# Kernel optimization log

Measured on AMD Instinct MI355X. Metric: run time of the kernel, lower is better.

Reference implementation:

```python
import jax, jax.numpy as jnp
import numpy as np

K_FRAC = 0.5  # matches init kwarg k


def setup_inputs() -> dict:
    key = jax.random.key(0)
    g = jax.random.normal(key, (16, 2048, 2048), dtype=jnp.float32)
    return {"g": g}


def reference(g):
    # k = int(N * k_frac): number of SMALLEST entries per row to zero out
    N = g.shape[-1]
    k = int(N * K_FRAC)
    g2 = g.reshape(-1, N)                       # [R, N]
    # indices of the k smallest values per row (topk of -g)
    _, idx = jax.lax.top_k(-g2, k)              # [R, k] int32
    rows = jnp.arange(g2.shape[0])[:, None]     # [R, 1]
    t = g2.at[rows, idx].set(0.0)               # scatter zeros at bottom-k positions
    return t.reshape(g.shape)
```

## Files before the change

### kernel.cpp

```cpp
#include <hip/hip_runtime.h>

#define ROW_N 2048
#define ROW_K 1024
#define HPAD  264
#define BUFA  528
#define BUFB  784
#define WHTOT 1040
#define WSTRIDE 1048

__device__ __forceinline__ void wfence() {
    asm volatile("s_waitcnt lgkmcnt(0)" ::: "memory");
}

__device__ __forceinline__ unsigned f2key(float x) {
    unsigned u = __float_as_uint(x);
    return u ^ ((unsigned)((int)u >> 31) | 0x80000000u);
}
__device__ __forceinline__ float key2f(unsigned k) {
    unsigned u = (k & 0x80000000u) ? (k ^ 0x80000000u) : ~k;
    return __uint_as_float(u);
}

__device__ __forceinline__ unsigned wave_incl_scan(unsigned x) {
    int v = (int)x;
    v += __builtin_amdgcn_update_dpp(0, v, 0x111, 0xf, 0xf, false);
    v += __builtin_amdgcn_update_dpp(0, v, 0x112, 0xf, 0xf, false);
    v += __builtin_amdgcn_update_dpp(0, v, 0x114, 0xf, 0xf, false);
    v += __builtin_amdgcn_update_dpp(0, v, 0x118, 0xf, 0xf, false);
    v += __builtin_amdgcn_update_dpp(0, v, 0x142, 0xa, 0xf, false);
    v += __builtin_amdgcn_update_dpp(0, v, 0x143, 0xc, 0xf, false);
    return (unsigned)v;
}

__device__ __forceinline__ void scan_pick(unsigned b0, unsigned b1, unsigned b2,
                                          unsigned b3, int lane, int rank_in,
                                          unsigned& digit, int& rank_out,
                                          int& cnteq_out) {
    unsigned s4 = b0 + b1 + b2 + b3;
    unsigned incl = wave_incl_scan(s4);
    int excl = (int)(incl - s4);
    bool found = (rank_in >= excl) && (rank_in < (int)incl);
    int rr = rank_in - excl;
    unsigned d = 4 * lane;
    unsigned beq = b0;
    if (found) {
        if (rr >= (int)b0) { rr -= (int)b0; d++; beq = b1;
            if (rr >= (int)b1) { rr -= (int)b1; d++; beq = b2;
                if (rr >= (int)b2) { rr -= (int)b2; d++; beq = b3; } } }
    }
    unsigned pack = (d << 24) | (beq << 12) | (unsigned)rr;
    unsigned long long bal = __ballot(found);
    int src = (int)__builtin_ctzll(bal);
    pack = (unsigned)__builtin_amdgcn_readlane((int)pack, src);
    digit = pack >> 24;
    cnteq_out = (int)((pack >> 12) & 0xfffu);
    rank_out = (int)(pack & 0xfffu);
}

__global__ __launch_bounds__(256)
void ktakes_kernel(const float* __restrict__ g, float* __restrict__ out) {
    const int tid  = threadIdx.x;
    const int wave = tid >> 6;
    const int lane = tid & 63;
    const int row  = blockIdx.x * 4 + wave;

    __shared__ unsigned H[4 * WSTRIDE];
    unsigned* hw   = H + wave * WSTRIDE;
    uint4*    hw4  = reinterpret_cast<uint4*>(hw);
    unsigned* hsub = hw + (lane & 1) * HPAD;

    const float4* g4 = reinterpret_cast<const float4*>(g + (size_t)row * ROW_N);
    float4*       o4 = reinterpret_cast<float4*>(out + (size_t)row * ROW_N);

    const uint4 z4 = {0u, 0u, 0u, 0u};
#pragma unroll
    for (int i = 0; i < 4; ++i) hw4[i * 64 + lane] = z4;
    if (lane < 16) hw[1024 + lane] = 0;

    unsigned k[32];
#pragma unroll
    for (int j = 0; j < 8; ++j) {
        float4 v = g4[j * 64 + lane];
        k[4*j+0] = f2key(v.x); k[4*j+1] = f2key(v.y);
        k[4*j+2] = f2key(v.z); k[4*j+3] = f2key(v.w);
    }

    unsigned prefix;
    int rank, cnteq;
    unsigned d;

    wfence();
#pragma unroll
    for (int c = 0; c < 32; ++c)
        atomicAdd(&hsub[k[c] >> 24], 1u);
    wfence();
    {
        uint4 h0 = *reinterpret_cast<const uint4*>(&hw[4 * lane]);
        uint4 h1 = *reinterpret_cast<const uint4*>(&hw[HPAD + 4 * lane]);
        scan_pick(h0.x + h1.x, h0.y + h1.y, h0.z + h1.z, h0.w + h1.w,
                  lane, ROW_K - 1, d, rank, cnteq);
        prefix = d << 24;
    }

#pragma unroll
    for (int c = 0; c < 32; ++c)
        if (((k[c] ^ prefix) >> 24) == 0)
            atomicAdd(&hw[BUFA + ((k[c] >> 16) & 255u)], 1u);
    wfence();
    {
        uint4 h = *reinterpret_cast<const uint4*>(&hw[BUFA + 4 * lane]);
        scan_pick(h.x, h.y, h.z, h.w, lane, rank, d, rank, cnteq);
        prefix |= d << 16;
    }

#pragma unroll
    for (int c = 0; c < 32; ++c)
        if (((k[c] ^ prefix) >> 16) == 0)
            atomicAdd(&hw[BUFB + ((k[c] >> 8) & 255u)], 1u);
    *reinterpret_cast<uint4*>(&hw[BUFA + 4 * lane]) = z4;
    wfence();
    {
        uint4 h = *reinterpret_cast<const uint4*>(&hw[BUFB + 4 * lane]);
        scan_pick(h.x, h.y, h.z, h.w, lane, rank, d, rank, cnteq);
        prefix |= d << 8;
    }

#pragma unroll
    for (int c = 0; c < 32; ++c)
        if (((k[c] ^ prefix) >> 8) == 0)
            atomicAdd(&hw[BUFA + (k[c] & 255u)], 1u);
    wfence();
    {
        uint4 h = *reinterpret_cast<const uint4*>(&hw[BUFA + 4 * lane]);
        scan_pick(h.x, h.y, h.z, h.w, lane, rank, d, rank, cnteq);
        prefix |= d;
    }

    const unsigned Kth = prefix;
    const int m = rank + 1;

    unsigned zm = 0;
    if (cnteq == m) {
#pragma unroll
        for (int c = 0; c < 32; ++c)
            if (k[c] <= Kth) zm |= 1u << c;
    } else {
        int base = 0;
#pragma unroll
        for (int j = 0; j < 8; ++j) {
            int eqmask = 0, e = 0;
#pragma unroll
            for (int c = 0; c < 4; ++c) {
                bool q = (k[4*j+c] == Kth);
                eqmask |= (int)q << c; e += (int)q;
            }
            int incl = e;
#pragma unroll
            for (int off = 1; off < 64; off <<= 1) {
                int n = __shfl_up(incl, off, 64);
                if (lane >= off) incl += n;
            }
            int excl = incl - e;
            int tot = __shfl(incl, 63, 64);
            int pos = base + excl;
#pragma unroll
            for (int c = 0; c < 4; ++c) {
                if (eqmask & (1 << c)) {
                    if (pos < m) zm |= 1u << (4*j+c);
                    pos++;
                }
            }
            base += tot;
        }
#pragma unroll
        for (int c = 0; c < 32; ++c)
            if (k[c] < Kth) zm |= 1u << c;
    }

#pragma unroll
    for (int j = 0; j < 8; ++j) {
        float4 v;
        v.x = (zm >> (4*j+0)) & 1u ? 0.0f : key2f(k[4*j+0]);
        v.y = (zm >> (4*j+1)) & 1u ? 0.0f : key2f(k[4*j+1]);
        v.z = (zm >> (4*j+2)) & 1u ? 0.0f : key2f(k[4*j+2]);
        v.w = (zm >> (4*j+3)) & 1u ? 0.0f : key2f(k[4*j+3]);
        o4[j * 64 + lane] = v;
    }
}

extern "C" void kernel_launch(void* const* d_in, const int* in_sizes, int n_in,
                              void* d_out, int out_size, void* d_ws, size_t ws_size,
                              hipStream_t stream) {
    const float* g = (const float*)d_in[0];
    float* out = (float*)d_out;
    const int rows = in_sizes[0] / ROW_N;
    hipLaunchKernelGGL(ktakes_kernel, dim3(rows / 4), dim3(256), 0, stream, g, out);
}
```

Baseline: 430.5 us.

## Use 10-bit first radix pass with candidate compaction and bitwise select

Replaces the four 8-bit radix histogram passes with a 1024-bin first pass over the top 10 key bits, using padded LDS indexing to spread bank conflicts. When the selected bin holds at most 128 candidates, they are compacted into LDS and the exact k-th key is found by a 22-step ballot-based bitwise selection instead of further histogram passes. Larger bins fall back to 8/8/6-bit histogram passes. Global loads are also issued before the histogram clear to overlap memory latency. The cost is a larger LDS footprint per wave and a data-dependent branch.

```diff
diff --git a/kernel.cpp b/kernel.cpp
--- a/kernel.cpp
+++ b/kernel.cpp
@@ -2,11 +2,9 @@
 
 #define ROW_N 2048
 #define ROW_K 1024
-#define HPAD  264
-#define BUFA  528
-#define BUFB  784
-#define WHTOT 1040
-#define WSTRIDE 1048
+#define HSIZE 1280
+#define LOFF  1280
+#define WSTRIDE 1416
 
 __device__ __forceinline__ void wfence() {
     asm volatile("s_waitcnt lgkmcnt(0)" ::: "memory");
@@ -19,6 +17,10 @@
 __device__ __forceinline__ float key2f(unsigned k) {
     unsigned u = (k & 0x80000000u) ? (k ^ 0x80000000u) : ~k;
     return __uint_as_float(u);
+}
+
+__device__ __forceinline__ unsigned pidx(unsigned bin) {
+    return bin + ((bin >> 4) << 2);
 }
 
 __device__ __forceinline__ unsigned wave_incl_scan(unsigned x) {
@@ -32,10 +34,10 @@
     return (unsigned)v;
 }
 
-__device__ __forceinline__ void scan_pick(unsigned b0, unsigned b1, unsigned b2,
-                                          unsigned b3, int lane, int rank_in,
-                                          unsigned& digit, int& rank_out,
-                                          int& cnteq_out) {
+__device__ __forceinline__ void scan_pick256(unsigned b0, unsigned b1, unsigned b2,
+                                             unsigned b3, int lane, int rank_in,
+                                             unsigned& digit, int& rank_out,
+                                             int& cnteq_out) {
     unsigned s4 = b0 + b1 + b2 + b3;
     unsigned incl = wave_incl_scan(s4);
     int excl = (int)(incl - s4);
@@ -65,79 +67,146 @@
     const int row  = blockIdx.x * 4 + wave;
 
     __shared__ unsigned H[4 * WSTRIDE];
-    unsigned* hw   = H + wave * WSTRIDE;
-    uint4*    hw4  = reinterpret_cast<uint4*>(hw);
-    unsigned* hsub = hw + (lane & 1) * HPAD;
+    unsigned* hw  = H + wave * WSTRIDE;
+    uint4*    hw4 = reinterpret_cast<uint4*>(hw);
+    unsigned* Lb  = hw + LOFF;
 
     const float4* g4 = reinterpret_cast<const float4*>(g + (size_t)row * ROW_N);
     float4*       o4 = reinterpret_cast<float4*>(out + (size_t)row * ROW_N);
 
+    float4 va[8];
+#pragma unroll
+    for (int j = 0; j < 8; ++j) va[j] = g4[j * 64 + lane];
     const uint4 z4 = {0u, 0u, 0u, 0u};
 #pragma unroll
-    for (int i = 0; i < 4; ++i) hw4[i * 64 + lane] = z4;
-    if (lane < 16) hw[1024 + lane] = 0;
+    for (int i = 0; i < 5; ++i) hw4[i * 64 + lane] = z4;
+    wfence();
 
     unsigned k[32];
 #pragma unroll
     for (int j = 0; j < 8; ++j) {
-        float4 v = g4[j * 64 + lane];
-        k[4*j+0] = f2key(v.x); k[4*j+1] = f2key(v.y);
-        k[4*j+2] = f2key(v.z); k[4*j+3] = f2key(v.w);
-    }
-
-    unsigned prefix;
-    int rank, cnteq;
-    unsigned d;
-
+        k[4*j+0] = f2key(va[j].x); k[4*j+1] = f2key(va[j].y);
+        k[4*j+2] = f2key(va[j].z); k[4*j+3] = f2key(va[j].w);
+        atomicAdd(&hw[pidx(k[4*j+0] >> 22)], 1u);
+        atomicAdd(&hw[pidx(k[4*j+1] >> 22)], 1u);
+        atomicAdd(&hw[pidx(k[4*j+2] >> 22)], 1u);
+        atomicAdd(&hw[pidx(k[4*j+3] >> 22)], 1u);
+    }
     wfence();
-#pragma unroll
-    for (int c = 0; c < 32; ++c)
-        atomicAdd(&hsub[k[c] >> 24], 1u);
-    wfence();
+
+    uint4 h0 = *reinterpret_cast<const uint4*>(&hw[20 * lane +  0]);
+    uint4 h1 = *reinterpret_cast<const uint4*>(&hw[20 * lane +  4]);
+    uint4 h2 = *reinterpret_cast<const uint4*>(&hw[20 * lane +  8]);
+    uint4 h3 = *reinterpret_cast<const uint4*>(&hw[20 * lane + 12]);
+    unsigned q0 = h0.x + h0.y + h0.z + h0.w;
+    unsigned q1 = h1.x + h1.y + h1.z + h1.w;
+    unsigned q2 = h2.x + h2.y + h2.z + h2.w;
+    unsigned q3 = h3.x + h3.y + h3.z + h3.w;
+    unsigned s16 = q0 + q1 + q2 + q3;
+    unsigned incl = wave_incl_scan(s16);
+    int excl = (int)(incl - s16);
+    bool found = (ROW_K - 1 >= excl) && (ROW_K - 1 < (int)incl);
+    int rr = (ROW_K - 1) - excl;
+    unsigned d = 16 * lane;
+    unsigned cnt = 0;
+    if (found) {
+        uint4 sel = h0;
+        if (rr >= (int)q0) { rr -= (int)q0; d += 4; sel = h1;
+            if (rr >= (int)q1) { rr -= (int)q1; d += 4; sel = h2;
+                if (rr >= (int)q2) { rr -= (int)q2; d += 4; sel = h3; } } }
+        cnt = sel.x;
+        if (rr >= (int)sel.x) { rr -= (int)sel.x; d++; cnt = sel.y;
+            if (rr >= (int)sel.y) { rr -= (int)sel.y; d++; cnt = sel.z;
+                if (rr >= (int)sel.z) { rr -= (int)sel.z; d++; cnt = sel.w; } } }
+    }
     {
-        uint4 h0 = *reinterpret_cast<const uint4*>(&hw[4 * lane]);
-        uint4 h1 = *reinterpret_cast<const uint4*>(&hw[HPAD + 4 * lane]);
-        scan_pick(h0.x + h1.x, h0.y + h1.y, h0.z + h1.z, h0.w + h1.w,
-                  lane, ROW_K - 1, d, rank, cnteq);
-        prefix = d << 24;
-    }
-
-#pragma unroll
-    for (int c = 0; c < 32; ++c)
-        if (((k[c] ^ prefix) >> 24) == 0)
-            atomicAdd(&hw[BUFA + ((k[c] >> 16) & 255u)], 1u);
-    wfence();
-    {
-        uint4 h = *reinterpret_cast<const uint4*>(&hw[BUFA + 4 * lane]);
-        scan_pick(h.x, h.y, h.z, h.w, lane, rank, d, rank, cnteq);
-        prefix |= d << 16;
-    }
-
-#pragma unroll
-    for (int c = 0; c < 32; ++c)
-        if (((k[c] ^ prefix) >> 16) == 0)
-            atomicAdd(&hw[BUFB + ((k[c] >> 8) & 255u)], 1u);
-    *reinterpret_cast<uint4*>(&hw[BUFA + 4 * lane]) = z4;
-    wfence();
-    {
-        uint4 h = *reinterpret_cast<const uint4*>(&hw[BUFB + 4 * lane]);
-        scan_pick(h.x, h.y, h.z, h.w, lane, rank, d, rank, cnteq);
-        prefix |= d << 8;
-    }
-
-#pragma unroll
-    for (int c = 0; c < 32; ++c)
-        if (((k[c] ^ prefix) >> 8) == 0)
-            atomicAdd(&hw[BUFA + (k[c] & 255u)], 1u);
-    wfence();
-    {
-        uint4 h = *reinterpret_cast<const uint4*>(&hw[BUFA + 4 * lane]);
-        scan_pick(h.x, h.y, h.z, h.w, lane, rank, d, rank, cnteq);
-        prefix |= d;
-    }
-
-    const unsigned Kth = prefix;
-    const int m = rank + 1;
+        unsigned long long bal = __ballot(found);
+        int src = (int)__builtin_ctzll(bal);
+        unsigned pA = (d << 12) | (unsigned)rr;
+        pA  = (unsigned)__shfl((int)pA, src, 64);
+        cnt = (unsigned)__shfl((int)cnt, src, 64);
+        d  = pA >> 12;
+        rr = (int)(pA & 0xfffu);
+    }
+    const int c1 = (int)cnt;
+    unsigned prefix = d << 22;
+    int rank = rr;
+
+    unsigned Kth;
+    int cnteq, m_rank;
+
+    if (c1 <= 128) {
+        unsigned base = 0;
+#pragma unroll
+        for (int c = 0; c < 32; ++c) {
+            bool mt = ((k[c] ^ prefix) >> 22) == 0;
+            unsigned long long bal = __ballot(mt);
+            if (mt) {
+                unsigned pos = base +
+                    (unsigned)__popcll(bal & ((1ull << lane) - 1ull));
+                Lb[pos] = k[c];
+            }
+            base += (unsigned)__popcll(bal);
+        }
+        wfence();
+        unsigned v0 = Lb[lane], v1 = Lb[64 + lane];
+        bool a0 = (lane < c1), a1 = (64 + lane < c1);
+        int r2 = rank;
+#pragma unroll
+        for (int bit = 21; bit >= 0; --bit) {
+            bool z0 = a0 && (((v0 >> bit) & 1u) == 0u);
+            bool z1 = a1 && (((v1 >> bit) & 1u) == 0u);
+            unsigned long long bz0 = __ballot(z0);
+            unsigned long long bz1 = __ballot(z1);
+            int nz = __popcll(bz0) + __popcll(bz1);
+            if (r2 < nz) { a0 = z0; a1 = z1; }
+            else         { r2 -= nz; a0 = a0 && !z0; a1 = a1 && !z1; }
+        }
+        unsigned long long ba0 = __ballot(a0);
+        unsigned long long ba1 = __ballot(a1);
+        cnteq = __popcll(ba0) + __popcll(ba1);
+        if (ba0) {
+            int src = (int)__builtin_ctzll(ba0);
+            Kth = (unsigned)__shfl((int)v0, src, 64);
+        } else {
+            int src = (int)__builtin_ctzll(ba1);
+            Kth = (unsigned)__shfl((int)v1, src, 64);
+        }
+        m_rank = r2;
+    } else {
+        unsigned dd;
+        hw4[lane] = z4; wfence();
+#pragma unroll
+        for (int c = 0; c < 32; ++c)
+            if (((k[c] ^ prefix) >> 22) == 0)
+                atomicAdd(&hw[(k[c] >> 14) & 255u], 1u);
+        wfence();
+        { uint4 h = hw4[lane];
+          scan_pick256(h.x, h.y, h.z, h.w, lane, rank, dd, rank, cnteq); }
+        prefix |= dd << 14;
+        hw4[lane] = z4; wfence();
+#pragma unroll
+        for (int c = 0; c < 32; ++c)
+            if (((k[c] ^ prefix) >> 14) == 0)
+                atomicAdd(&hw[(k[c] >> 6) & 255u], 1u);
+        wfence();
+        { uint4 h = hw4[lane];
+          scan_pick256(h.x, h.y, h.z, h.w, lane, rank, dd, rank, cnteq); }
+        prefix |= dd << 6;
+        hw4[lane] = z4; wfence();
+#pragma unroll
+        for (int c = 0; c < 32; ++c)
+            if (((k[c] ^ prefix) >> 6) == 0)
+                atomicAdd(&hw[k[c] & 63u], 1u);
+        wfence();
+        { uint4 h = hw4[lane];
+          scan_pick256(h.x, h.y, h.z, h.w, lane, rank, dd, rank, cnteq); }
+        prefix |= dd;
+        Kth = prefix;
+        m_rank = rank;
+    }
+
+    const int m = m_rank + 1;
 
     unsigned zm = 0;
     if (cnteq == m) {
@@ -154,15 +223,15 @@
                 bool q = (k[4*j+c] == Kth);
                 eqmask |= (int)q << c; e += (int)q;
             }
-            int incl = e;
+            int incl2 = e;
 #pragma unroll
             for (int off = 1; off < 64; off <<= 1) {
-                int n = __shfl_up(incl, off, 64);
-                if (lane >= off) incl += n;
-            }
-            int excl = incl - e;
-            int tot = __shfl(incl, 63, 64);
-            int pos = base + excl;
+                int n = __shfl_up(incl2, off, 64);
+                if (lane >= off) incl2 += n;
+            }
+            int excl2 = incl2 - e;
+            int tot = __shfl(incl2, 63, 64);
+            int pos = base + excl2;
 #pragma unroll
             for (int c = 0; c < 4; ++c) {
                 if (eqmask & (1 << c)) {
```

Result: no change. 438.7 us (+1.9%).
